# Performance work log

Hardware: AMD Instinct MI355X
Metric: run time of the kernel (lower is better)

Reference implementation:

```python
import jax, jax.numpy as jnp
import numpy as np

C, T, H, W, K = 12, 10, 4, 7, 3  # hardcoded in the original forward
PAD = 1
EPS = 1e-5


def setup_inputs() -> dict:
    key = jax.random.key(0)
    ks = jax.random.split(key, 14)
    nt = 32768
    x = jax.random.normal(ks[0], (nt, C, T, H * W), jnp.float32)
    # G: Linear(T -> 2T) -> BN1d(2T) -> ReLU -> Linear(2T -> K) -> Softmax
    w_g1 = jax.random.normal(ks[1], (2 * T, T), jnp.float32) * 0.3
    g1_gamma = 1.0 + 0.1 * jax.random.normal(ks[2], (2 * T,), jnp.float32)
    g1_beta = 0.1 * jax.random.normal(ks[3], (2 * T,), jnp.float32)
    g1_mean = 0.1 * jax.random.normal(ks[4], (2 * T,), jnp.float32)
    g1_var = jax.random.uniform(ks[5], (2 * T,), jnp.float32, 0.5, 1.5)
    w_g2 = jax.random.normal(ks[6], (K, 2 * T), jnp.float32) * 0.3
    # L: Conv1d(C -> C//4, K) -> BN1d(C//4) -> ReLU -> Conv1d(C//4 -> C, 1) -> Sigmoid
    w_l1 = jax.random.normal(ks[7], (C // 4, C, K), jnp.float32) * 0.3
    l1_gamma = 1.0 + 0.1 * jax.random.normal(ks[8], (C // 4,), jnp.float32)
    l1_beta = 0.1 * jax.random.normal(ks[9], (C // 4,), jnp.float32)
    l1_mean = 0.1 * jax.random.normal(ks[10], (C // 4,), jnp.float32)
    l1_var = jax.random.uniform(ks[11], (C // 4,), jnp.float32, 0.5, 1.5)
    w_l2 = jax.random.normal(ks[12], (C, C // 4, 1), jnp.float32) * 0.3
    return dict(x=x, w_g1=w_g1, g1_gamma=g1_gamma, g1_beta=g1_beta,
                g1_mean=g1_mean, g1_var=g1_var, w_g2=w_g2, w_l1=w_l1,
                l1_gamma=l1_gamma, l1_beta=l1_beta, l1_mean=l1_mean,
                l1_var=l1_var, w_l2=w_l2)


def reference(x, w_g1, g1_gamma, g1_beta, g1_mean, g1_var, w_g2,
              w_l1, l1_gamma, l1_beta, l1_mean, l1_var, w_l2):
    n = x.shape[0]
    new_x = x.reshape(n, C, T, H, W)
    # adaptive_avg_pool2d((1,1)) == mean over spatial dims -> [n, C, T]
    pooled = new_x.mean(axis=(3, 4))
    # --- G branch: per-(sample,channel) temporal kernel, [n, C, K] ---
    rows = pooled.reshape(n * C, T)
    z = rows @ w_g1.T
    z = (z - g1_mean) * jax.lax.rsqrt(g1_var + EPS) * g1_gamma + g1_beta
    z = jax.nn.relu(z)
    kern = jax.nn.softmax(z @ w_g2.T, axis=-1).reshape(n, C, K)
    # --- L branch: local channel-temporal gating, [n, C, T] ---
    a = jax.lax.conv_general_dilated(pooled, w_l1, (1,), [(K // 2, K // 2)],
                                     dimension_numbers=('NCH', 'OIH', 'NCH'))
    a = (a - l1_mean[None, :, None]) * jax.lax.rsqrt(l1_var + EPS)[None, :, None] \
        * l1_gamma[None, :, None] + l1_beta[None, :, None]
    a = jax.nn.relu(a)
    a = jax.lax.conv_general_dilated(a, w_l2, (1,), [(0, 0)],
                                     dimension_numbers=('NCH', 'OIH', 'NCH'))
    act = jax.nn.sigmoid(a)  # [n, C, T]
    # --- modulate and apply per-(sample,channel) depthwise temporal conv ---
    xm = new_x * act[:, :, :, None, None]  # [n, C, T, H, W]
    xp = jnp.pad(xm, ((0, 0), (0, 0), (PAD, PAD), (0, 0), (0, 0)))
    out = kern[:, :, 0, None, None, None] * xp[:, :, 0:T]
    for j in range(1, K):  # K=3, tiny structural loop
        out = out + kern[:, :, j, None, None, None] * xp[:, :, j:j + T]
    # permute [n,c,t,h,w] -> [n,t,c,h,w] and flatten time into batch
    out = jnp.transpose(out, (0, 2, 1, 3, 4)).reshape(n * T, C, H, W)
    return out
```

## Files before the change

kernel.cpp:

```cpp
#include <hip/hip_runtime.h>


#define CC 12
#define TT 10
#define HWS 28
#define KK 3
#define CT (CC*TT)
#define SAMPLE (CC*TT*HWS)
#define SAMPLE4 (SAMPLE/4)
#define CHW4 (CC*HWS/4)
#define HW4 (HWS/4)
#define EPSF 1e-5f

typedef float f4 __attribute__((ext_vector_type(4)));

__global__ __launch_bounds__(256, 8) void tam_kernel(
    const float* __restrict__ x,
    const float* __restrict__ w_g1,
    const float* __restrict__ g1_gamma, const float* __restrict__ g1_beta,
    const float* __restrict__ g1_mean,  const float* __restrict__ g1_var,
    const float* __restrict__ w_g2,
    const float* __restrict__ w_l1,
    const float* __restrict__ l1_gamma, const float* __restrict__ l1_beta,
    const float* __restrict__ l1_mean,  const float* __restrict__ l1_var,
    const float* __restrict__ w_l2,
    float* __restrict__ out)
{
    __shared__ float sx[SAMPLE];
    __shared__ float spool[CT];
    __shared__ float sz[CC * 2 * TT];
    __shared__ float skern[CC * KK];
    __shared__ float sa1[3 * TT];
    __shared__ float sact[CT];

    const int n   = blockIdx.x;
    const int tid = threadIdx.x;

    const f4* xg  = reinterpret_cast<const f4*>(x + (size_t)n * SAMPLE);
    f4* sx4 = reinterpret_cast<f4*>(sx);
    for (int v = tid; v < SAMPLE4; v += 256) {
        const int c   = v / (TT * HW4);
        const int rem = v % (TT * HW4);
        const int t   = rem / HW4;
        const int i   = rem % HW4;
        const f4 val = __builtin_nontemporal_load(xg + v);
        sx4[t * CHW4 + c * HW4 + i] = val;
    }
    __syncthreads();

    if (tid < CT) {
        const int c = tid / TT, t = tid % TT;
        const f4* row = sx4 + t * CHW4 + c * HW4;
        f4 a = row[0];
        #pragma unroll
        for (int i = 1; i < HW4; ++i) { const f4 b = row[i]; a.x+=b.x; a.y+=b.y; a.z+=b.z; a.w+=b.w; }
        spool[tid] = (a.x + a.y + a.z + a.w) * (1.0f / 28.0f);
    }
    __syncthreads();

    if (tid < CC * 2 * TT) {
        const int c = tid / (2 * TT), j = tid % (2 * TT);
        float s = 0.f;
        #pragma unroll
        for (int t = 0; t < TT; ++t) s += spool[c * TT + t] * w_g1[j * TT + t];
        s = (s - g1_mean[j]) * rsqrtf(g1_var[j] + EPSF) * g1_gamma[j] + g1_beta[j];
        sz[tid] = fmaxf(s, 0.f);
    } else {
        const int idx2 = tid - CC * 2 * TT;
        #pragma unroll
        for (int q = 0; q < 2; ++q) {
            const int e = idx2 * 2 + q;
            if (e < 3 * TT) {
                const int m = e / TT, t = e % TT;
                float s = 0.f;
                #pragma unroll
                for (int c = 0; c < CC; ++c) {
                    #pragma unroll
                    for (int k = 0; k < KK; ++k) {
                        const int t2 = t + k - 1;
                        if (t2 >= 0 && t2 < TT)
                            s += spool[c * TT + t2] * w_l1[(m * CC + c) * KK + k];
                    }
                }
                s = (s - l1_mean[m]) * rsqrtf(l1_var[m] + EPSF) * l1_gamma[m] + l1_beta[m];
                sa1[e] = fmaxf(s, 0.f);
            }
        }
    }
    __syncthreads();

    if (tid < CC) {
        const int c = tid;
        float sc0 = 0.f, sc1 = 0.f, sc2 = 0.f;
        #pragma unroll
        for (int j = 0; j < 2 * TT; ++j) {
            const float zj = sz[c * 2 * TT + j];
            sc0 += zj * w_g2[0 * 2 * TT + j];
            sc1 += zj * w_g2[1 * 2 * TT + j];
            sc2 += zj * w_g2[2 * 2 * TT + j];
        }
        const float m = fmaxf(sc0, fmaxf(sc1, sc2));
        const float e0 = __expf(sc0 - m), e1 = __expf(sc1 - m), e2 = __expf(sc2 - m);
        const float r = 1.0f / (e0 + e1 + e2);
        skern[c * KK + 0] = e0 * r;
        skern[c * KK + 1] = e1 * r;
        skern[c * KK + 2] = e2 * r;
    }
    if (tid >= 64 && tid < 64 + CT) {
        const int idx = tid - 64;
        const int c = idx / TT, t = idx % TT;
        float s = 0.f;
        #pragma unroll
        for (int m = 0; m < 3; ++m) s += sa1[m * TT + t] * w_l2[c * 3 + m];
        sact[idx] = 1.0f / (1.0f + __expf(-s));
    }
    __syncthreads();

    f4* og4 = reinterpret_cast<f4*>(out + (size_t)n * SAMPLE);
    for (int v = tid; v < SAMPLE4; v += 256) {
        const int t   = v / CHW4;
        const int c   = (v % CHW4) / HW4;
        const float k0 = skern[c * KK + 0];
        const float k1 = skern[c * KK + 1];
        const float k2 = skern[c * KK + 2];
        f4 acc = (f4)0.f;
        if (t > 0) {
            const float a = sact[c * TT + (t - 1)] * k0;
            const f4 xv = sx4[v - CHW4];
            acc += a * xv;
        }
        {
            const float a = sact[c * TT + t] * k1;
            const f4 xv = sx4[v];
            acc += a * xv;
        }
        if (t < TT - 1) {
            const float a = sact[c * TT + (t + 1)] * k2;
            const f4 xv = sx4[v + CHW4];
            acc += a * xv;
        }
        __builtin_nontemporal_store(acc, og4 + v);
    }
}

extern "C" void kernel_launch(void* const* d_in, const int* in_sizes, int n_in,
                              void* d_out, int out_size, void* d_ws, size_t ws_size,
                              hipStream_t stream) {
    (void)n_in; (void)out_size; (void)d_ws; (void)ws_size;
    const float* x        = (const float*)d_in[0];
    const float* w_g1     = (const float*)d_in[1];
    const float* g1_gamma = (const float*)d_in[2];
    const float* g1_beta  = (const float*)d_in[3];
    const float* g1_mean  = (const float*)d_in[4];
    const float* g1_var   = (const float*)d_in[5];
    const float* w_g2     = (const float*)d_in[6];
    const float* w_l1     = (const float*)d_in[7];
    const float* l1_gamma = (const float*)d_in[8];
    const float* l1_beta  = (const float*)d_in[9];
    const float* l1_mean  = (const float*)d_in[10];
    const float* l1_var   = (const float*)d_in[11];
    const float* w_l2     = (const float*)d_in[12];
    float* out = (float*)d_out;

    const int n_total = in_sizes[0] / SAMPLE;
    tam_kernel<<<n_total, 256, 0, stream>>>(
        x, w_g1, g1_gamma, g1_beta, g1_mean, g1_var, w_g2,
        w_l1, l1_gamma, l1_beta, l1_mean, l1_var, w_l2, out);
}
```

Measured before the change: 223.0 us.

## Run each sample on a single wavefront, replacing block barriers with LDS waits

The block shrinks from 256 threads to a single 64-lane wavefront per sample, so every __syncthreads becomes an lgkmcnt wait plus a scheduling barrier. The whole sample is loaded into registers with 13+1 unrolled vector loads, and the shared-memory copy keeps the original [c,t,hw] order instead of being transposed. The per-(c,t) gate and softmax kernel weights are folded into a precomputed f4 table, and the output loop is unrolled with clamped neighbour indices so it has no branches. This trades more serial work per thread, and fewer threads to hide latency, for removing block-level barrier overhead. The output store also drops the nontemporal hint.

```diff
diff --git a/kernel.cpp b/kernel.cpp
--- a/kernel.cpp
+++ b/kernel.cpp
@@ -4,17 +4,16 @@
 #define CC 12
 #define TT 10
 #define HWS 28
-#define KK 3
-#define CT (CC*TT)
-#define SAMPLE (CC*TT*HWS)
-#define SAMPLE4 (SAMPLE/4)
-#define CHW4 (CC*HWS/4)
-#define HW4 (HWS/4)
+#define SAMPLE 3360
+#define SAMPLE4 840
 #define EPSF 1e-5f
 
 typedef float f4 __attribute__((ext_vector_type(4)));
 
-__global__ __launch_bounds__(256, 8) void tam_kernel(
+#define WSYNC() do { asm volatile("s_waitcnt lgkmcnt(0)" ::: "memory"); \
+                     __builtin_amdgcn_sched_barrier(0); } while (0)
+
+__global__ __launch_bounds__(64) void tam_kernel(
     const float* __restrict__ x,
     const float* __restrict__ w_g1,
     const float* __restrict__ g1_gamma, const float* __restrict__ g1_beta,
@@ -26,120 +25,135 @@
     const float* __restrict__ w_l2,
     float* __restrict__ out)
 {
-    __shared__ float sx[SAMPLE];
-    __shared__ float spool[CT];
+    __shared__ f4    sx4[SAMPLE4];
+    __shared__ float spool[CC * TT];
     __shared__ float sz[CC * 2 * TT];
-    __shared__ float skern[CC * KK];
     __shared__ float sa1[3 * TT];
-    __shared__ float sact[CT];
+    __shared__ f4    skern[CC];
+    __shared__ float sact[CC * TT];
+    __shared__ f4    sw4[CC * TT];
 
-    const int n   = blockIdx.x;
-    const int tid = threadIdx.x;
+    const int n    = blockIdx.x;
+    const int lane = threadIdx.x;
 
-    const f4* xg  = reinterpret_cast<const f4*>(x + (size_t)n * SAMPLE);
-    f4* sx4 = reinterpret_cast<f4*>(sx);
-    for (int v = tid; v < SAMPLE4; v += 256) {
-        const int c   = v / (TT * HW4);
-        const int rem = v % (TT * HW4);
-        const int t   = rem / HW4;
-        const int i   = rem % HW4;
-        const f4 val = __builtin_nontemporal_load(xg + v);
-        sx4[t * CHW4 + c * HW4 + i] = val;
-    }
-    __syncthreads();
+    const f4* xg = reinterpret_cast<const f4*>(x + (size_t)n * SAMPLE);
+    f4 r[13];
+    #pragma unroll
+    for (int k = 0; k < 13; ++k)
+        r[k] = __builtin_nontemporal_load(xg + k * 64 + lane);
+    f4 rt = (f4)0.f;
+    if (lane < 8) rt = __builtin_nontemporal_load(xg + 832 + lane);
+    #pragma unroll
+    for (int k = 0; k < 13; ++k) sx4[k * 64 + lane] = r[k];
+    if (lane < 8) sx4[832 + lane] = rt;
+    WSYNC();
 
-    if (tid < CT) {
-        const int c = tid / TT, t = tid % TT;
-        const f4* row = sx4 + t * CHW4 + c * HW4;
-        f4 a = row[0];
-        #pragma unroll
-        for (int i = 1; i < HW4; ++i) { const f4 b = row[i]; a.x+=b.x; a.y+=b.y; a.z+=b.z; a.w+=b.w; }
-        spool[tid] = (a.x + a.y + a.z + a.w) * (1.0f / 28.0f);
-    }
-    __syncthreads();
-
-    if (tid < CC * 2 * TT) {
-        const int c = tid / (2 * TT), j = tid % (2 * TT);
-        float s = 0.f;
-        #pragma unroll
-        for (int t = 0; t < TT; ++t) s += spool[c * TT + t] * w_g1[j * TT + t];
-        s = (s - g1_mean[j]) * rsqrtf(g1_var[j] + EPSF) * g1_gamma[j] + g1_beta[j];
-        sz[tid] = fmaxf(s, 0.f);
-    } else {
-        const int idx2 = tid - CC * 2 * TT;
-        #pragma unroll
-        for (int q = 0; q < 2; ++q) {
-            const int e = idx2 * 2 + q;
-            if (e < 3 * TT) {
-                const int m = e / TT, t = e % TT;
-                float s = 0.f;
-                #pragma unroll
-                for (int c = 0; c < CC; ++c) {
-                    #pragma unroll
-                    for (int k = 0; k < KK; ++k) {
-                        const int t2 = t + k - 1;
-                        if (t2 >= 0 && t2 < TT)
-                            s += spool[c * TT + t2] * w_l1[(m * CC + c) * KK + k];
-                    }
-                }
-                s = (s - l1_mean[m]) * rsqrtf(l1_var[m] + EPSF) * l1_gamma[m] + l1_beta[m];
-                sa1[e] = fmaxf(s, 0.f);
-            }
+    #pragma unroll
+    for (int rr = 0; rr < 2; ++rr) {
+        const int row = lane + rr * 64;
+        if (row < CC * TT) {
+            const f4* rp = sx4 + row * 7;
+            f4 a = rp[0];
+            #pragma unroll
+            for (int i = 1; i < 7; ++i) a += rp[i];
+            spool[row] = (a.x + a.y + a.z + a.w) * (1.0f / 28.0f);
         }
     }
-    __syncthreads();
+    WSYNC();
 
-    if (tid < CC) {
-        const int c = tid;
+    #pragma unroll
+    for (int q = 0; q < 5; ++q) {
+        const int task = lane + q * 64;
+        if (task < 240) {
+            const int c = task / 20, j = task % 20;
+            float s = 0.f;
+            #pragma unroll
+            for (int t = 0; t < TT; ++t) s += spool[c * TT + t] * w_g1[j * TT + t];
+            s = (s - g1_mean[j]) * rsqrtf(g1_var[j] + EPSF) * g1_gamma[j] + g1_beta[j];
+            sz[task] = fmaxf(s, 0.f);
+        } else if (task < 270) {
+            const int e = task - 240;
+            const int m = e / TT, t = e % TT;
+            float s = 0.f;
+            #pragma unroll
+            for (int c = 0; c < CC; ++c) {
+                #pragma unroll
+                for (int k = 0; k < 3; ++k) {
+                    const int t2 = t + k - 1;
+                    if (t2 >= 0 && t2 < TT)
+                        s += spool[c * TT + t2] * w_l1[(m * CC + c) * 3 + k];
+                }
+            }
+            s = (s - l1_mean[m]) * rsqrtf(l1_var[m] + EPSF) * l1_gamma[m] + l1_beta[m];
+            sa1[e] = fmaxf(s, 0.f);
+        }
+    }
+    WSYNC();
+
+    if (lane < CC) {
+        const int c = lane;
         float sc0 = 0.f, sc1 = 0.f, sc2 = 0.f;
         #pragma unroll
-        for (int j = 0; j < 2 * TT; ++j) {
-            const float zj = sz[c * 2 * TT + j];
-            sc0 += zj * w_g2[0 * 2 * TT + j];
-            sc1 += zj * w_g2[1 * 2 * TT + j];
-            sc2 += zj * w_g2[2 * 2 * TT + j];
+        for (int j = 0; j < 20; ++j) {
+            const float zj = sz[c * 20 + j];
+            sc0 += zj * w_g2[j];
+            sc1 += zj * w_g2[20 + j];
+            sc2 += zj * w_g2[40 + j];
         }
-        const float m = fmaxf(sc0, fmaxf(sc1, sc2));
-        const float e0 = __expf(sc0 - m), e1 = __expf(sc1 - m), e2 = __expf(sc2 - m);
-        const float r = 1.0f / (e0 + e1 + e2);
-        skern[c * KK + 0] = e0 * r;
-        skern[c * KK + 1] = e1 * r;
-        skern[c * KK + 2] = e2 * r;
+        const float mx = fmaxf(sc0, fmaxf(sc1, sc2));
+        const float e0 = __expf(sc0 - mx), e1 = __expf(sc1 - mx), e2 = __expf(sc2 - mx);
+        const float ri = 1.0f / (e0 + e1 + e2);
+        f4 kk; kk.x = e0 * ri; kk.y = e1 * ri; kk.z = e2 * ri; kk.w = 0.f;
+        skern[c] = kk;
     }
-    if (tid >= 64 && tid < 64 + CT) {
-        const int idx = tid - 64;
-        const int c = idx / TT, t = idx % TT;
-        float s = 0.f;
-        #pragma unroll
-        for (int m = 0; m < 3; ++m) s += sa1[m * TT + t] * w_l2[c * 3 + m];
-        sact[idx] = 1.0f / (1.0f + __expf(-s));
+    #pragma unroll
+    for (int q = 0; q < 2; ++q) {
+        const int task = lane + q * 64;
+        if (task < CC * TT) {
+            const int c = task / TT, t = task % TT;
+            float s = 0.f;
+            #pragma unroll
+            for (int m = 0; m < 3; ++m) s += sa1[m * TT + t] * w_l2[c * 3 + m];
+            sact[task] = 1.0f / (1.0f + __expf(-s));
+        }
     }
-    __syncthreads();
+    WSYNC();
 
-    f4* og4 = reinterpret_cast<f4*>(out + (size_t)n * SAMPLE);
-    for (int v = tid; v < SAMPLE4; v += 256) {
-        const int t   = v / CHW4;
-        const int c   = (v % CHW4) / HW4;
-        const float k0 = skern[c * KK + 0];
-        const float k1 = skern[c * KK + 1];
-        const float k2 = skern[c * KK + 2];
-        f4 acc = (f4)0.f;
-        if (t > 0) {
-            const float a = sact[c * TT + (t - 1)] * k0;
-            const f4 xv = sx4[v - CHW4];
-            acc += a * xv;
+    #pragma unroll
+    for (int q = 0; q < 2; ++q) {
+        const int task = lane + q * 64;
+        if (task < CC * TT) {
+            const int c = task / TT, t = task % TT;
+            const f4 kk = skern[c];
+            f4 w;
+            w.x = (t > 0) ? kk.x * sact[c * TT + t - 1] : 0.f;
+            w.y = kk.y * sact[c * TT + t];
+            w.z = (t < 9) ? kk.z * sact[c * TT + t + 1] : 0.f;
+            w.w = 0.f;
+            sw4[task] = w;
         }
-        {
-            const float a = sact[c * TT + t] * k1;
-            const f4 xv = sx4[v];
-            acc += a * xv;
+    }
+    WSYNC();
+
+    f4* og = reinterpret_cast<f4*>(out + (size_t)n * SAMPLE);
+    #pragma unroll
+    for (int k = 0; k < 14; ++k) {
+        const int vo = lane + k * 64;
+        if (k < 13 || lane < 8) {
+            const int t   = vo / 84;
+            const int rem = vo % 84;
+            const int c   = rem / 7;
+            const int s4  = rem % 7;
+            const f4 w = sw4[c * TT + t];
+            const int base = c * 70 + s4;
+            const int tm = (t > 0) ? t - 1 : 0;
+            const int tp = (t < 9) ? t + 1 : 9;
+            const f4 x0 = sx4[base + tm * 7];
+            const f4 x1 = sx4[base + t * 7];
+            const f4 x2 = sx4[base + tp * 7];
+            const f4 acc = w.x * x0 + w.y * x1 + w.z * x2;
+            og[vo] = acc;
         }
-        if (t < TT - 1) {
-            const float a = sact[c * TT + (t + 1)] * k2;
-            const f4 xv = sx4[v + CHW4];
-            acc += a * xv;
-        }
-        __builtin_nontemporal_store(acc, og4 + v);
     }
 }
 
@@ -163,7 +177,7 @@
     float* out = (float*)d_out;
 
     const int n_total = in_sizes[0] / SAMPLE;
-    tam_kernel<<<n_total, 256, 0, stream>>>(
+    tam_kernel<<<n_total, 64, 0, stream>>>(
         x, w_g1, g1_gamma, g1_beta, g1_mean, g1_var, w_g2,
         w_l1, l1_gamma, l1_beta, l1_mean, l1_var, w_l2, out);
 }
```

Result: slower. 238.4 us (+6.9%).
